# Kernel tuning notes

Hardware: AMD Instinct MI355X
Metric: run time of the kernel (lower is better)

## Reference

```python
import jax, jax.numpy as jnp
import numpy as np

B, P, M, W = 32, 4096, 12, 9
IN_C, OUT_C = 64, 64
IN_PN_PAD = P + 1  # in_point_num + 1 padding row


def setup_inputs() -> dict:
    key = jax.random.key(0)
    k1, k2, k3, k4 = jax.random.split(key, 4)
    in_pc_pad = jax.random.normal(k1, (B, IN_PN_PAD, IN_C), dtype=jnp.float32)
    weights = jax.random.normal(k2, (W, OUT_C * IN_C), dtype=jnp.float32)
    bias = jnp.zeros((OUT_C,), dtype=jnp.float32)
    w_weights = jax.random.normal(k3, (P, M, W), dtype=jnp.float32) / (9.0 * W)
    neighbor_id_lstlst = jax.random.randint(k4, (P, M), 0, IN_PN_PAD, dtype=jnp.int64)
    neighbor_mask_lst = jnp.ones((P, M), dtype=jnp.float32)
    return {
        "in_pc_pad": in_pc_pad,
        "weights": weights,
        "bias": bias,
        "w_weights": w_weights,
        "neighbor_id_lstlst": neighbor_id_lstlst,
        "neighbor_mask_lst": neighbor_mask_lst,
    }


def reference(in_pc_pad, weights, bias, w_weights, neighbor_id_lstlst, neighbor_mask_lst):
    # gather neighbor features: [B, P, M, IN_C]
    in_neighbors = in_pc_pad[:, neighbor_id_lstlst]
    # mask the per-(point,neighbor) basis coefficients: [P, M, W]
    w2 = w_weights * neighbor_mask_lst[:, :, None]
    # synthesize per-(point,neighbor) weight matrices from basis: [P, M, OUT_C, IN_C]
    wmat = jnp.einsum('pmw,wc->pmc', w2, weights).reshape(P, M, OUT_C, IN_C)
    # batched matvec + neighbor-sum reduce (fused over m): [B, P, OUT_C]
    out_pc = jnp.einsum('pmoi,bpmi->bpo', wmat, in_neighbors)
    return out_pc + bias
```

## Files before the change

kernel.cpp:

```cpp
#include <hip/hip_runtime.h>

#define NB 32
#define NP 4096
#define NM 12
#define NW 9
#define NC 64
#define PN_PAD 4097
#define KDIM (NW * NC)
#define NKS (KDIM / 16)
#define KCH 4
#define KSPC (NKS / KCH)
#define AROW 584

#define WSW_BYTES (KDIM * NC * 2)
#define W2_OFFSET WSW_BYTES
#define W2_BYTES (NP * NM * 12 * 4)
#define XB_OFFSET (W2_OFFSET + W2_BYTES)
#define XB_BYTES (NB * PN_PAD * NC * 2)
#define WS_NEED ((size_t)XB_OFFSET + XB_BYTES)

typedef __attribute__((ext_vector_type(8))) short short8;
typedef __attribute__((ext_vector_type(2))) float float2v;
typedef __attribute__((ext_vector_type(4))) float float4v;
typedef __attribute__((ext_vector_type(16))) float float16v;

#define PK_FMA_LO(acc, x, wp)                                                  \
    asm("v_pk_fma_f32 %0, %1, %2, %0 op_sel:[0,0,0] op_sel_hi:[1,0,1]"         \
        : "+v"(acc) : "v"(x), "s"(wp))
#define PK_FMA_HI(acc, x, wp)                                                  \
    asm("v_pk_fma_f32 %0, %1, %2, %0 op_sel:[0,1,0] op_sel_hi:[1,1,1]"         \
        : "+v"(acc) : "v"(x), "s"(wp))

__device__ __forceinline__ unsigned short f32_to_bf16(float f) {
    union { float f; unsigned u; } v; v.f = f;
    unsigned r = v.u + 0x7FFFu + ((v.u >> 16) & 1u);
    return (unsigned short)(r >> 16);
}

__device__ __forceinline__ uint2 pack_bf16x4(float4v v) {
    union { float f; unsigned u; } a0, a1, a2, a3;
    a0.f = v[0]; a1.f = v[1]; a2.f = v[2]; a3.f = v[3];
    unsigned u0 = a0.u + 0x8000u, u1 = a1.u + 0x8000u;
    unsigned u2 = a2.u + 0x8000u, u3 = a3.u + 0x8000u;
    uint2 r;
    r.x = __builtin_amdgcn_perm(u1, u0, 0x07060302u);
    r.y = __builtin_amdgcn_perm(u3, u2, 0x07060302u);
    return r;
}

__device__ __forceinline__ uint2 pack_bf16x4_2(float2v lo, float2v hi) {
    union { float f; unsigned u; } a0, a1, a2, a3;
    a0.f = lo[0]; a1.f = lo[1]; a2.f = hi[0]; a3.f = hi[1];
    unsigned u0 = a0.u + 0x8000u, u1 = a1.u + 0x8000u;
    unsigned u2 = a2.u + 0x8000u, u3 = a3.u + 0x8000u;
    uint2 r;
    r.x = __builtin_amdgcn_perm(u1, u0, 0x07060302u);
    r.y = __builtin_amdgcn_perm(u3, u2, 0x07060302u);
    return r;
}

__device__ __forceinline__ void bf16x4_to_2xf2(uint2 u, float2v& lo, float2v& hi) {
    union { unsigned u; float f; } c0, c1, c2, c3;
    c0.u = u.x << 16; c1.u = u.x & 0xFFFF0000u;
    c2.u = u.y << 16; c3.u = u.y & 0xFFFF0000u;
    lo = (float2v){c0.f, c1.f};
    hi = (float2v){c2.f, c3.f};
}

template<int DOX>
__global__ void prep_all(const float* __restrict__ w,
                         const float* __restrict__ ww,
                         const float* __restrict__ mask,
                         const float* __restrict__ x,
                         unsigned short* __restrict__ wsw,
                         float* __restrict__ w2d,
                         unsigned short* __restrict__ xb) {
    int idx = blockIdx.x * 256 + threadIdx.x;
    if (idx < KDIM * NC) {
        int j    = idx & 7;
        int lane = (idx >> 3) & 63;
        int f    = idx >> 9;
        int nt2  = f & 1;
        int ks   = f >> 1;
        int k = ks * 16 + ((lane >> 5) * 8) + j;
        int n = nt2 * 32 + (lane & 31);
        int wi = k >> 6;
        int ii = k & 63;
        wsw[idx] = f32_to_bf16(w[wi * (NC * NC) + n * NC + ii]);
    }
    if (idx < NP * NM * 12) {
        int wq = idx % 12;
        int pm = idx / 12;
        float v = 0.f;
        if (wq < NW) v = ww[pm * NW + wq] * mask[pm];
        w2d[idx] = v;
    }
    if (DOX) {
        const int n4 = NB * PN_PAD * NC / 4;
        if (idx < n4) {
            const float4v* x4 = (const float4v*)x;
            ((uint2*)xb)[idx] = pack_bf16x4(x4[idx]);
        }
    }
}

template<int BF16X>
__global__ __launch_bounds__(512)
void conv_main(const float* __restrict__ x,
               const unsigned short* __restrict__ xb,
               const unsigned short* __restrict__ wsw,
               const float* __restrict__ bias,
               const float* __restrict__ w2d,
               const int* __restrict__ nid,
               float* __restrict__ out) {
    __shared__ __align__(16) unsigned short A[NB * AROW];

    const int p = blockIdx.x;
    const int tid = threadIdx.x;

    {
        const int i4 = tid & 15;
        const int b  = tid >> 4;
        const float2v* w2pv = (const float2v*)(w2d + p * (NM * 12));
        const int* nidp = nid + p * NM;

        int nm[NM];
        #pragma unroll
        for (int m = 0; m < NM; ++m) nm[m] = nidp[m];

        float2v acc0[NW], acc1[NW];
        #pragma unroll
        for (int w = 0; w < NW; ++w) {
            acc0[w] = (float2v){0.f, 0.f};
            acc1[w] = (float2v){0.f, 0.f};
        }

        if (BF16X) {
            const uint2* xb2 = (const uint2*)xb;
            uint2 xv[NM];
            #pragma unroll
            for (int m = 0; m < NM; ++m)
                xv[m] = xb2[(b * PN_PAD + nm[m]) * 16 + i4];
            #pragma unroll
            for (int m = 0; m < NM; ++m) {
                float2v lo, hi;
                bf16x4_to_2xf2(xv[m], lo, hi);
                #pragma unroll
                for (int j = 0; j < 4; ++j) {
                    const float2v wp = w2pv[m * 6 + j];
                    PK_FMA_LO(acc0[2 * j],     lo, wp);
                    PK_FMA_LO(acc1[2 * j],     hi, wp);
                    PK_FMA_HI(acc0[2 * j + 1], lo, wp);
                    PK_FMA_HI(acc1[2 * j + 1], hi, wp);
                }
                const float2v wp8 = w2pv[m * 6 + 4];
                PK_FMA_LO(acc0[8], lo, wp8);
                PK_FMA_LO(acc1[8], hi, wp8);
            }
        } else {
            const float4v* x4 = (const float4v*)x;
            float4v xv[NM];
            #pragma unroll
            for (int m = 0; m < NM; ++m)
                xv[m] = x4[(b * PN_PAD + nm[m]) * 16 + i4];
            #pragma unroll
            for (int m = 0; m < NM; ++m) {
                const float2v lo = {xv[m][0], xv[m][1]};
                const float2v hi = {xv[m][2], xv[m][3]};
                #pragma unroll
                for (int j = 0; j < 4; ++j) {
                    const float2v wp = w2pv[m * 6 + j];
                    PK_FMA_LO(acc0[2 * j],     lo, wp);
                    PK_FMA_LO(acc1[2 * j],     hi, wp);
                    PK_FMA_HI(acc0[2 * j + 1], lo, wp);
                    PK_FMA_HI(acc1[2 * j + 1], hi, wp);
                }
                const float2v wp8 = w2pv[m * 6 + 4];
                PK_FMA_LO(acc0[8], lo, wp8);
                PK_FMA_LO(acc1[8], hi, wp8);
            }
        }

        #pragma unroll
        for (int w = 0; w < NW; ++w)
            *(uint2*)&A[b * AROW + w * 64 + i4 * 4] = pack_bf16x4_2(acc0[w], acc1[w]);
    }
    __syncthreads();

    {
        const int lane = tid & 63;
        const int wid  = tid >> 6;
        const int nt   = wid & 1;
        const int kc   = wid >> 1;
        const int col  = lane & 31;
        const int hf   = lane >> 5;

        float16v acc = {0.f,0.f,0.f,0.f, 0.f,0.f,0.f,0.f,
                        0.f,0.f,0.f,0.f, 0.f,0.f,0.f,0.f};
        const short8* Bfrags = (const short8*)wsw;

        #pragma unroll
        for (int s = 0; s < KSPC; ++s) {
            const int ks = kc * KSPC + s;
            short8 bfrag = Bfrags[(ks * 2 + nt) * 64 + lane];
            const short8 a = *(const short8*)&A[col * AROW + ks * 16 + hf * 8];
            acc = __builtin_amdgcn_mfma_f32_32x32x16_bf16(a, bfrag, acc, 0, 0, 0);
        }
        __syncthreads();

        float* P = (float*)A;
        #pragma unroll
        for (int reg = 0; reg < 16; ++reg) {
            const int row = (reg & 3) + 8 * (reg >> 2) + 4 * hf;
            P[((nt * KCH + kc) * 32 + row) * 32 + col] = acc[reg];
        }
        __syncthreads();

        const int c  = tid & 31;
        const int rg = (tid >> 5) & 7;
        const int t2 = tid >> 8;
        const int o  = t2 * 32 + c;
        const float bv = bias[o];
        #pragma unroll
        for (int rr = 0; rr < 4; ++rr) {
            const int r = rg * 4 + rr;
            const float s = P[((t2 * KCH + 0) * 32 + r) * 32 + c]
                          + P[((t2 * KCH + 1) * 32 + r) * 32 + c]
                          + P[((t2 * KCH + 2) * 32 + r) * 32 + c]
                          + P[((t2 * KCH + 3) * 32 + r) * 32 + c];
            out[(r * NP + p) * NC + o] = s + bv;
        }
    }
}

extern "C" void kernel_launch(void* const* d_in, const int* in_sizes, int n_in,
                              void* d_out, int out_size, void* d_ws, size_t ws_size,
                              hipStream_t stream) {
    const float* x    = (const float*)d_in[0];
    const float* w    = (const float*)d_in[1];
    const float* bias = (const float*)d_in[2];
    const float* ww   = (const float*)d_in[3];
    const int*   nid  = (const int*)d_in[4];
    const float* mask = (const float*)d_in[5];
    float* out = (float*)d_out;
    unsigned short* wsw = (unsigned short*)d_ws;
    float* w2d = (float*)((char*)d_ws + W2_OFFSET);
    unsigned short* xb = (unsigned short*)((char*)d_ws + XB_OFFSET);

    if (ws_size >= WS_NEED) {
        const int n4 = NB * PN_PAD * NC / 4;
        hipLaunchKernelGGL(prep_all<1>, dim3((n4 + 255) / 256), dim3(256), 0, stream,
                           w, ww, mask, x, wsw, w2d, xb);
        hipLaunchKernelGGL(conv_main<1>, dim3(NP), dim3(512), 0, stream,
                           x, xb, wsw, bias, w2d, nid, out);
    } else {
        const int prep_elems = NP * NM * 12;
        hipLaunchKernelGGL(prep_all<0>, dim3((prep_elems + 255) / 256), dim3(256), 0, stream,
                           w, ww, mask, x, wsw, w2d, xb);
        hipLaunchKernelGGL(conv_main<0>, dim3(NP), dim3(512), 0, stream,
                           x, xb, wsw, bias, w2d, nid, out);
    }
}
```

Before: 132.5 us.

## Process eight points per block with prefetched gathers and LDS-staged basis weights

The main kernel now loops over eight consecutive points per block instead of one. Each point's neighbour gathers are issued while the MFMA stage of the previous point runs, so gather latency overlaps compute. The per-point basis coefficients for all eight points are staged once in LDS and read as vector operands, replacing the scalar-operand path. Blocks drop from 4096 to 512 and occupancy is requested at four blocks per CU, which may leave the GPU under-filled and adds a barrier per point.

Result: slower. 141.3 us (+6.7%).

```diff
diff --git a/kernel.cpp b/kernel.cpp
--- a/kernel.cpp
+++ b/kernel.cpp
@@ -11,10 +11,13 @@
 #define KCH 4
 #define KSPC (NKS / KCH)
 #define AROW 584
+#define PPB 8
+#define NBLK (NP / PPB)
+#define WROW 144
 
 #define WSW_BYTES (KDIM * NC * 2)
 #define W2_OFFSET WSW_BYTES
-#define W2_BYTES (NP * NM * 12 * 4)
+#define W2_BYTES (NP * WROW * 4)
 #define XB_OFFSET (W2_OFFSET + W2_BYTES)
 #define XB_BYTES (NB * PN_PAD * NC * 2)
 #define WS_NEED ((size_t)XB_OFFSET + XB_BYTES)
@@ -26,10 +29,10 @@
 
 #define PK_FMA_LO(acc, x, wp)                                                  \
     asm("v_pk_fma_f32 %0, %1, %2, %0 op_sel:[0,0,0] op_sel_hi:[1,0,1]"         \
-        : "+v"(acc) : "v"(x), "s"(wp))
+        : "+v"(acc) : "v"(x), "v"(wp))
 #define PK_FMA_HI(acc, x, wp)                                                  \
     asm("v_pk_fma_f32 %0, %1, %2, %0 op_sel:[0,1,0] op_sel_hi:[1,1,1]"         \
-        : "+v"(acc) : "v"(x), "s"(wp))
+        : "+v"(acc) : "v"(x), "v"(wp))
 
 __device__ __forceinline__ unsigned short f32_to_bf16(float f) {
     union { float f; unsigned u; } v; v.f = f;
@@ -105,7 +108,7 @@
 }
 
 template<int BF16X>
-__global__ __launch_bounds__(512)
+__global__ __launch_bounds__(512, 4)
 void conv_main(const float* __restrict__ x,
                const unsigned short* __restrict__ xb,
                const unsigned short* __restrict__ wsw,
@@ -114,91 +117,112 @@
                const int* __restrict__ nid,
                float* __restrict__ out) {
     __shared__ __align__(16) unsigned short A[NB * AROW];
-
-    const int p = blockIdx.x;
+    __shared__ __align__(16) float Wlds[PPB * WROW];
+
     const int tid = threadIdx.x;
-
+    const int p0  = blockIdx.x * PPB;
+
+    const int i4 = tid & 15;
+    const int b  = tid >> 4;
+    const int lane = tid & 63;
+    const int wid  = tid >> 6;
+    const int nt   = wid & 1;
+    const int kc   = wid >> 1;
+    const int col  = lane & 31;
+    const int hf   = lane >> 5;
+    const int rc  = tid & 31;
+    const int rg  = (tid >> 5) & 7;
+    const int t2  = tid >> 8;
+
+    const short8* Bfrags = (const short8*)wsw;
+    const uint2*  xb2    = (const uint2*)xb;
+    const float4v* x4    = (const float4v*)x;
+
+    int     nmv[NM];
+    uint2   xv[NM];
+    float4v xvf[NM];
     {
-        const int i4 = tid & 15;
-        const int b  = tid >> 4;
-        const float2v* w2pv = (const float2v*)(w2d + p * (NM * 12));
-        const int* nidp = nid + p * NM;
-
-        int nm[NM];
-        #pragma unroll
-        for (int m = 0; m < NM; ++m) nm[m] = nidp[m];
-
+        const float* wsrc = w2d + (size_t)p0 * WROW;
+        #pragma unroll
+        for (int i = 0; i < 3; ++i) {
+            int j = tid + i * 512;
+            if (j < PPB * WROW) Wlds[j] = wsrc[j];
+        }
+        const int4* np4 = (const int4*)(nid + p0 * NM);
+        int4 nr0 = np4[0], nr1 = np4[1], nr2 = np4[2];
+        nmv[0]=__builtin_amdgcn_readfirstlane(nr0.x); nmv[1]=__builtin_amdgcn_readfirstlane(nr0.y);
+        nmv[2]=__builtin_amdgcn_readfirstlane(nr0.z); nmv[3]=__builtin_amdgcn_readfirstlane(nr0.w);
+        nmv[4]=__builtin_amdgcn_readfirstlane(nr1.x); nmv[5]=__builtin_amdgcn_readfirstlane(nr1.y);
+        nmv[6]=__builtin_amdgcn_readfirstlane(nr1.z); nmv[7]=__builtin_amdgcn_readfirstlane(nr1.w);
+        nmv[8]=__builtin_amdgcn_readfirstlane(nr2.x); nmv[9]=__builtin_amdgcn_readfirstlane(nr2.y);
+        nmv[10]=__builtin_amdgcn_readfirstlane(nr2.z); nmv[11]=__builtin_amdgcn_readfirstlane(nr2.w);
+        #pragma unroll
+        for (int m = 0; m < NM; ++m) {
+            if (BF16X) xv[m]  = xb2[(b * PN_PAD + nmv[m]) * 16 + i4];
+            else       xvf[m] = x4 [(b * PN_PAD + nmv[m]) * 16 + i4];
+        }
+    }
+    __syncthreads();
+
+    for (int it = 0; it < PPB; ++it) {
+        const int p = p0 + it;
+        const int havenext = (it + 1 < PPB);
+
+        int4 nr0, nr1, nr2;
+        if (havenext) {
+            const int4* np4 = (const int4*)(nid + (p + 1) * NM);
+            nr0 = np4[0]; nr1 = np4[1]; nr2 = np4[2];
+        }
+
+        const float2v* Wl = (const float2v*)(Wlds + it * WROW);
         float2v acc0[NW], acc1[NW];
         #pragma unroll
         for (int w = 0; w < NW; ++w) {
             acc0[w] = (float2v){0.f, 0.f};
             acc1[w] = (float2v){0.f, 0.f};
         }
-
-        if (BF16X) {
-            const uint2* xb2 = (const uint2*)xb;
-            uint2 xv[NM];
+        #pragma unroll
+        for (int m = 0; m < NM; ++m) {
+            float2v lo, hi;
+            if (BF16X) bf16x4_to_2xf2(xv[m], lo, hi);
+            else { lo = (float2v){xvf[m][0], xvf[m][1]}; hi = (float2v){xvf[m][2], xvf[m][3]}; }
             #pragma unroll
-            for (int m = 0; m < NM; ++m)
-                xv[m] = xb2[(b * PN_PAD + nm[m]) * 16 + i4];
+            for (int j = 0; j < 4; ++j) {
+                const float2v wp = Wl[m * 6 + j];
+                PK_FMA_LO(acc0[2 * j],     lo, wp);
+                PK_FMA_LO(acc1[2 * j],     hi, wp);
+                PK_FMA_HI(acc0[2 * j + 1], lo, wp);
+                PK_FMA_HI(acc1[2 * j + 1], hi, wp);
+            }
+            const float2v wp8 = Wl[m * 6 + 4];
+            PK_FMA_LO(acc0[8], lo, wp8);
+            PK_FMA_LO(acc1[8], hi, wp8);
+        }
+
+        __syncthreads();
+
+        #pragma unroll
+        for (int w = 0; w < NW; ++w)
+            *(uint2*)&A[b * AROW + w * 64 + i4 * 4] = pack_bf16x4_2(acc0[w], acc1[w]);
+
+        if (havenext) {
+            nmv[0]=__builtin_amdgcn_readfirstlane(nr0.x); nmv[1]=__builtin_amdgcn_readfirstlane(nr0.y);
+            nmv[2]=__builtin_amdgcn_readfirstlane(nr0.z); nmv[3]=__builtin_amdgcn_readfirstlane(nr0.w);
+            nmv[4]=__builtin_amdgcn_readfirstlane(nr1.x); nmv[5]=__builtin_amdgcn_readfirstlane(nr1.y);
+            nmv[6]=__builtin_amdgcn_readfirstlane(nr1.z); nmv[7]=__builtin_amdgcn_readfirstlane(nr1.w);
+            nmv[8]=__builtin_amdgcn_readfirstlane(nr2.x); nmv[9]=__builtin_amdgcn_readfirstlane(nr2.y);
+            nmv[10]=__builtin_amdgcn_readfirstlane(nr2.z); nmv[11]=__builtin_amdgcn_readfirstlane(nr2.w);
             #pragma unroll
             for (int m = 0; m < NM; ++m) {
-                float2v lo, hi;
-                bf16x4_to_2xf2(xv[m], lo, hi);
-                #pragma unroll
-                for (int j = 0; j < 4; ++j) {
-                    const float2v wp = w2pv[m * 6 + j];
-                    PK_FMA_LO(acc0[2 * j],     lo, wp);
-                    PK_FMA_LO(acc1[2 * j],     hi, wp);
-                    PK_FMA_HI(acc0[2 * j + 1], lo, wp);
-                    PK_FMA_HI(acc1[2 * j + 1], hi, wp);
-                }
-                const float2v wp8 = w2pv[m * 6 + 4];
-                PK_FMA_LO(acc0[8], lo, wp8);
-                PK_FMA_LO(acc1[8], hi, wp8);
+                if (BF16X) xv[m]  = xb2[(b * PN_PAD + nmv[m]) * 16 + i4];
+                else       xvf[m] = x4 [(b * PN_PAD + nmv[m]) * 16 + i4];
             }
-        } else {
-            const float4v* x4 = (const float4v*)x;
-            float4v xv[NM];
-            #pragma unroll
-            for (int m = 0; m < NM; ++m)
-                xv[m] = x4[(b * PN_PAD + nm[m]) * 16 + i4];
-            #pragma unroll
-            for (int m = 0; m < NM; ++m) {
-                const float2v lo = {xv[m][0], xv[m][1]};
-                const float2v hi = {xv[m][2], xv[m][3]};
-                #pragma unroll
-                for (int j = 0; j < 4; ++j) {
-                    const float2v wp = w2pv[m * 6 + j];
-                    PK_FMA_LO(acc0[2 * j],     lo, wp);
-                    PK_FMA_LO(acc1[2 * j],     hi, wp);
-                    PK_FMA_HI(acc0[2 * j + 1], lo, wp);
-                    PK_FMA_HI(acc1[2 * j + 1], hi, wp);
-                }
-                const float2v wp8 = w2pv[m * 6 + 4];
-                PK_FMA_LO(acc0[8], lo, wp8);
-                PK_FMA_LO(acc1[8], hi, wp8);
-            }
-        }
-
-        #pragma unroll
-        for (int w = 0; w < NW; ++w)
-            *(uint2*)&A[b * AROW + w * 64 + i4 * 4] = pack_bf16x4_2(acc0[w], acc1[w]);
-    }
-    __syncthreads();
-
-    {
-        const int lane = tid & 63;
-        const int wid  = tid >> 6;
-        const int nt   = wid & 1;
-        const int kc   = wid >> 1;
-        const int col  = lane & 31;
-        const int hf   = lane >> 5;
+        }
+
+        __syncthreads();
 
         float16v acc = {0.f,0.f,0.f,0.f, 0.f,0.f,0.f,0.f,
                         0.f,0.f,0.f,0.f, 0.f,0.f,0.f,0.f};
-        const short8* Bfrags = (const short8*)wsw;
-
         #pragma unroll
         for (int s = 0; s < KSPC; ++s) {
             const int ks = kc * KSPC + s;
@@ -216,18 +240,15 @@
         }
         __syncthreads();
 
-        const int c  = tid & 31;
-        const int rg = (tid >> 5) & 7;
-        const int t2 = tid >> 8;
-        const int o  = t2 * 32 + c;
+        const int o  = t2 * 32 + rc;
         const float bv = bias[o];
         #pragma unroll
         for (int rr = 0; rr < 4; ++rr) {
             const int r = rg * 4 + rr;
-            const float s = P[((t2 * KCH + 0) * 32 + r) * 32 + c]
-                          + P[((t2 * KCH + 1) * 32 + r) * 32 + c]
-                          + P[((t2 * KCH + 2) * 32 + r) * 32 + c]
-                          + P[((t2 * KCH + 3) * 32 + r) * 32 + c];
+            const float s = P[((t2 * KCH + 0) * 32 + r) * 32 + rc]
+                          + P[((t2 * KCH + 1) * 32 + r) * 32 + rc]
+                          + P[((t2 * KCH + 2) * 32 + r) * 32 + rc]
+                          + P[((t2 * KCH + 3) * 32 + r) * 32 + rc];
             out[(r * NP + p) * NC + o] = s + bv;
         }
     }
@@ -251,13 +272,13 @@
         const int n4 = NB * PN_PAD * NC / 4;
         hipLaunchKernelGGL(prep_all<1>, dim3((n4 + 255) / 256), dim3(256), 0, stream,
                            w, ww, mask, x, wsw, w2d, xb);
-        hipLaunchKernelGGL(conv_main<1>, dim3(NP), dim3(512), 0, stream,
+        hipLaunchKernelGGL(conv_main<1>, dim3(NBLK), dim3(512), 0, stream,
                            x, xb, wsw, bias, w2d, nid, out);
     } else {
         const int prep_elems = NP * NM * 12;
         hipLaunchKernelGGL(prep_all<0>, dim3((prep_elems + 255) / 256), dim3(256), 0, stream,
                            w, ww, mask, x, wsw, w2d, xb);
-        hipLaunchKernelGGL(conv_main<0>, dim3(NP), dim3(512), 0, stream,
+        hipLaunchKernelGGL(conv_main<0>, dim3(NBLK), dim3(512), 0, stream,
                            x, xb, wsw, bias, w2d, nid, out);
     }
 }
```
